# Kernel optimization log

Hardware: AMD Instinct MI355X
Metric: run time of the kernel (lower is better)

Reference implementation:

```python
import jax, jax.numpy as jnp
import numpy as np

def setup_inputs() -> dict:
    key = jax.random.key(0)
    k1, k2 = jax.random.split(key)
    B, S, D, R = 16, 1024, 1024, 128
    batch = jax.random.normal(k1, (B, S, D), dtype=jnp.float32)
    # probe parameter initialized uniform(-0.05, 0.05) as in the torch module
    proj = jax.random.uniform(k2, (D, R), dtype=jnp.float32, minval=-0.05, maxval=0.05)
    return {"batch": batch, "proj": proj}

def reference(batch, proj):
    # transformed: [B, S, R]
    t = jnp.matmul(batch, proj)
    # squared L2 distances for all pairs: ||t_i||^2 + ||t_j||^2 - 2 t_i . t_j
    sq_norms = jnp.sum(t * t, axis=-1)                      # [B, S]
    cross = jnp.einsum('bir,bjr->bij', t, t)                # [B, S, S]
    d = sq_norms[:, :, None] + sq_norms[:, None, :] - 2.0 * cross
    return jnp.maximum(d, 0.0)  # clamp tiny negative values from the identity
```

## Files before the change

### kernel.cpp

```cpp
#include <hip/hip_runtime.h>

typedef __attribute__((ext_vector_type(8))) __bf16 bf16x8;
typedef __attribute__((ext_vector_type(4))) float f32x4;

#define B_ 16
#define S_ 1024
#define D_ 1024
#define R_ 128

__global__ __launch_bounds__(256) void k_transpose(const float* __restrict__ proj,
                                                   __bf16* __restrict__ projT) {
    __shared__ __bf16 tile[64][66];
    const int k0 = blockIdx.x * 64;
    const int r0 = blockIdx.y * 64;
#pragma unroll
    for (int it = 0; it < 16; ++it) {
        int idx = it * 256 + threadIdx.x;
        int kk = idx >> 6, rr = idx & 63;
        tile[kk][rr] = (__bf16)proj[(size_t)(k0 + kk) * R_ + (r0 + rr)];
    }
    __syncthreads();
#pragma unroll
    for (int it = 0; it < 16; ++it) {
        int idx = it * 256 + threadIdx.x;
        int rr = idx >> 6, kk = idx & 63;
        projT[(size_t)(r0 + rr) * D_ + (k0 + kk)] = tile[kk][rr];
    }
}

__global__ __launch_bounds__(256, 4) void k_proj(const float* __restrict__ batch,
                                                 const __bf16* __restrict__ projT,
                                                 __bf16* __restrict__ t,
                                                 float* __restrict__ sqn) {
    const int wave = threadIdx.x >> 6;
    const int lane = threadIdx.x & 63;
    const int ln = lane & 15;
    const int q  = lane >> 4;
    const int m0 = blockIdx.x * 16;
    const int kbase = wave * 256;
    const float* arow = batch + (size_t)(m0 + ln) * D_ + kbase;

    f32x4 acc[8];
#pragma unroll
    for (int ni = 0; ni < 8; ++ni) acc[ni] = f32x4{0.f, 0.f, 0.f, 0.f};

#pragma unroll 4
    for (int k0 = 0; k0 < 256; k0 += 32) {
        const int ka = k0 + q * 8;
        float4 alo = *(const float4*)(arow + ka);
        float4 ahi = *(const float4*)(arow + ka + 4);
        bf16x8 af;
        af[0] = (__bf16)alo.x; af[1] = (__bf16)alo.y;
        af[2] = (__bf16)alo.z; af[3] = (__bf16)alo.w;
        af[4] = (__bf16)ahi.x; af[5] = (__bf16)ahi.y;
        af[6] = (__bf16)ahi.z; af[7] = (__bf16)ahi.w;
#pragma unroll
        for (int ni = 0; ni < 8; ++ni) {
            bf16x8 bf = *(const bf16x8*)(projT + (size_t)(ni * 16 + ln) * D_ + kbase + ka);
            acc[ni] = __builtin_amdgcn_mfma_f32_16x16x32_bf16(af, bf, acc[ni], 0, 0, 0);
        }
    }

    __shared__ f32x4 red[4][8][64];
    __shared__ float sqpart[4][16];
#pragma unroll
    for (int ni = 0; ni < 8; ++ni) red[wave][ni][lane] = acc[ni];
    __syncthreads();

    float sq[4] = {0.f, 0.f, 0.f, 0.f};
#pragma unroll
    for (int p = 0; p < 2; ++p) {
        const int ni = wave * 2 + p;
        f32x4 v = red[0][ni][lane];
#pragma unroll
        for (int w = 1; w < 4; ++w) {
            f32x4 u = red[w][ni][lane];
            v[0] += u[0]; v[1] += u[1]; v[2] += u[2]; v[3] += u[3];
        }
#pragma unroll
        for (int r = 0; r < 4; ++r) {
            __bf16 h = (__bf16)v[r];
            t[(size_t)(m0 + q * 4 + r) * R_ + ni * 16 + ln] = h;
            float f = (float)h;
            sq[r] += f * f;
        }
    }
#pragma unroll
    for (int r = 0; r < 4; ++r) {
#pragma unroll
        for (int off = 1; off < 16; off <<= 1)
            sq[r] += __shfl_xor(sq[r], off, 64);
    }
    if (ln == 0) {
#pragma unroll
        for (int r = 0; r < 4; ++r) sqpart[wave][q * 4 + r] = sq[r];
    }
    __syncthreads();
    if (threadIdx.x < 16) {
        float s = sqpart[0][threadIdx.x] + sqpart[1][threadIdx.x] +
                  sqpart[2][threadIdx.x] + sqpart[3][threadIdx.x];
        sqn[m0 + threadIdx.x] = s;
    }
}

__global__ __launch_bounds__(256) void k_gram(const __bf16* __restrict__ t,
                                              const float* __restrict__ sqn,
                                              float* __restrict__ out) {
    const int b = blockIdx.z;
    const int wave = threadIdx.x >> 6;
    const int lane = threadIdx.x & 63;
    const int ln = lane & 15;
    const int q  = lane >> 4;
    const int wi = wave >> 1, wj = wave & 1;
    const int i0 = blockIdx.y * 128 + wi * 64;
    const int j0 = blockIdx.x * 128 + wj * 64;
    const __bf16* tb = t + (size_t)b * S_ * R_;
    const float* sqb = sqn + (size_t)b * S_;

    f32x4 acc[4][4];
#pragma unroll
    for (int mi = 0; mi < 4; ++mi)
#pragma unroll
        for (int ni = 0; ni < 4; ++ni) acc[mi][ni] = f32x4{0.f, 0.f, 0.f, 0.f};

#pragma unroll
    for (int k0 = 0; k0 < R_; k0 += 32) {
        const int ka = k0 + q * 8;
        bf16x8 af[4], bfm[4];
#pragma unroll
        for (int mi = 0; mi < 4; ++mi)
            af[mi] = *(const bf16x8*)(tb + (size_t)(i0 + mi * 16 + ln) * R_ + ka);
#pragma unroll
        for (int ni = 0; ni < 4; ++ni)
            bfm[ni] = *(const bf16x8*)(tb + (size_t)(j0 + ni * 16 + ln) * R_ + ka);
#pragma unroll
        for (int mi = 0; mi < 4; ++mi)
#pragma unroll
            for (int ni = 0; ni < 4; ++ni)
                acc[mi][ni] = __builtin_amdgcn_mfma_f32_16x16x32_bf16(
                    af[mi], bfm[ni], acc[mi][ni], 0, 0, 0);
    }

    float sqj[4];
#pragma unroll
    for (int ni = 0; ni < 4; ++ni) sqj[ni] = sqb[j0 + ni * 16 + ln];

    float* outb = out + (size_t)b * S_ * S_;
#pragma unroll
    for (int mi = 0; mi < 4; ++mi) {
#pragma unroll
        for (int r = 0; r < 4; ++r) {
            const int i = i0 + mi * 16 + q * 4 + r;
            const float si = sqb[i];
            float* orow = outb + (size_t)i * S_ + j0;
#pragma unroll
            for (int ni = 0; ni < 4; ++ni) {
                float v = si + sqj[ni] - 2.f * acc[mi][ni][r];
                orow[ni * 16 + ln] = fmaxf(v, 0.f);
            }
        }
    }
}

extern "C" void kernel_launch(void* const* d_in, const int* in_sizes, int n_in,
                              void* d_out, int out_size, void* d_ws, size_t ws_size,
                              hipStream_t stream) {
    const float* batch = (const float*)d_in[0];
    const float* proj  = (const float*)d_in[1];
    float* out = (float*)d_out;

    char* ws = (char*)d_ws;
    __bf16* t     = (__bf16*)ws;
    __bf16* projT = (__bf16*)(ws + (size_t)B_ * S_ * R_ * 2);
    float*  sqn   = (float*)(ws + (size_t)B_ * S_ * R_ * 2
                                + (size_t)R_ * D_ * 2);

    k_transpose<<<dim3(D_ / 64, R_ / 64), 256, 0, stream>>>(proj, projT);
    k_proj<<<dim3((B_ * S_) / 16), 256, 0, stream>>>(batch, projT, t, sqn);
    k_gram<<<dim3(S_ / 128, S_ / 128, B_), 256, 0, stream>>>(t, sqn, out);
}
```

Measured before the change: 156.8 us.

## Stage projection inputs through LDS and write gram output transposed as float4

In k_proj, each wave now loads its 16x256 fp32 slice of batch with row-contiguous float4 loads, converts it to bf16 and stages it in shared memory. The MFMA A fragments are then read from LDS, replacing strided per-lane global loads. The reduction buffers reuse the same LDS allocation. k_gram relies on the symmetry of the distance matrix to store each accumulator's four values as one float4 into the transposed position, and gains a launch-bounds occupancy hint; this cuts store instruction count but changes the write access pattern.

Result: no change. 157.5 us (+0.5%).

```diff
diff --git a/kernel.cpp b/kernel.cpp
--- a/kernel.cpp
+++ b/kernel.cpp
@@ -1,6 +1,7 @@
 #include <hip/hip_runtime.h>
 
 typedef __attribute__((ext_vector_type(8))) __bf16 bf16x8;
+typedef __attribute__((ext_vector_type(4))) __bf16 bf16x4;
 typedef __attribute__((ext_vector_type(4))) float f32x4;
 
 #define B_ 16
@@ -28,6 +29,7 @@
     }
 }
 
+#define STG_LD 264
 __global__ __launch_bounds__(256, 4) void k_proj(const float* __restrict__ batch,
                                                  const __bf16* __restrict__ projT,
                                                  __bf16* __restrict__ t,
@@ -38,22 +40,27 @@
     const int q  = lane >> 4;
     const int m0 = blockIdx.x * 16;
     const int kbase = wave * 256;
-    const float* arow = batch + (size_t)(m0 + ln) * D_ + kbase;
+
+    __shared__ __align__(16) char smraw[4 * 16 * STG_LD * 2];
+    __bf16 (*stg)[STG_LD] =
+        reinterpret_cast<__bf16(*)[STG_LD]>(smraw + wave * (16 * STG_LD * 2));
+
+    const float* abase = batch + (size_t)m0 * D_ + kbase;
+#pragma unroll
+    for (int r = 0; r < 16; ++r) {
+        float4 v = *(const float4*)(abase + (size_t)r * D_ + lane * 4);
+        bf16x4 h = {(__bf16)v.x, (__bf16)v.y, (__bf16)v.z, (__bf16)v.w};
+        *(bf16x4*)&stg[r][lane * 4] = h;
+    }
 
     f32x4 acc[8];
 #pragma unroll
     for (int ni = 0; ni < 8; ++ni) acc[ni] = f32x4{0.f, 0.f, 0.f, 0.f};
 
-#pragma unroll 4
+#pragma unroll
     for (int k0 = 0; k0 < 256; k0 += 32) {
         const int ka = k0 + q * 8;
-        float4 alo = *(const float4*)(arow + ka);
-        float4 ahi = *(const float4*)(arow + ka + 4);
-        bf16x8 af;
-        af[0] = (__bf16)alo.x; af[1] = (__bf16)alo.y;
-        af[2] = (__bf16)alo.z; af[3] = (__bf16)alo.w;
-        af[4] = (__bf16)ahi.x; af[5] = (__bf16)ahi.y;
-        af[6] = (__bf16)ahi.z; af[7] = (__bf16)ahi.w;
+        bf16x8 af = *(const bf16x8*)&stg[ln][ka];
 #pragma unroll
         for (int ni = 0; ni < 8; ++ni) {
             bf16x8 bf = *(const bf16x8*)(projT + (size_t)(ni * 16 + ln) * D_ + kbase + ka);
@@ -61,20 +68,21 @@
         }
     }
 
-    __shared__ f32x4 red[4][8][64];
-    __shared__ float sqpart[4][16];
+    __syncthreads();
+    f32x4 (*red)[64] = reinterpret_cast<f32x4(*)[64]>(smraw);
+    float (*sqpart)[16] = reinterpret_cast<float(*)[16]>(smraw + 32768);
 #pragma unroll
-    for (int ni = 0; ni < 8; ++ni) red[wave][ni][lane] = acc[ni];
+    for (int ni = 0; ni < 8; ++ni) red[wave * 8 + ni][lane] = acc[ni];
     __syncthreads();
 
     float sq[4] = {0.f, 0.f, 0.f, 0.f};
 #pragma unroll
     for (int p = 0; p < 2; ++p) {
         const int ni = wave * 2 + p;
-        f32x4 v = red[0][ni][lane];
+        f32x4 v = red[ni][lane];
 #pragma unroll
         for (int w = 1; w < 4; ++w) {
-            f32x4 u = red[w][ni][lane];
+            f32x4 u = red[w * 8 + ni][lane];
             v[0] += u[0]; v[1] += u[1]; v[2] += u[2]; v[3] += u[3];
         }
 #pragma unroll
@@ -103,9 +111,9 @@
     }
 }
 
-__global__ __launch_bounds__(256) void k_gram(const __bf16* __restrict__ t,
-                                              const float* __restrict__ sqn,
-                                              float* __restrict__ out) {
+__global__ __launch_bounds__(256, 4) void k_gram(const __bf16* __restrict__ t,
+                                                 const float* __restrict__ sqn,
+                                                 float* __restrict__ out) {
     const int b = blockIdx.z;
     const int wave = threadIdx.x >> 6;
     const int lane = threadIdx.x & 63;
@@ -148,16 +156,16 @@
     float* outb = out + (size_t)b * S_ * S_;
 #pragma unroll
     for (int mi = 0; mi < 4; ++mi) {
+        float4 si4 = *(const float4*)(sqb + i0 + mi * 16 + q * 4);
 #pragma unroll
-        for (int r = 0; r < 4; ++r) {
-            const int i = i0 + mi * 16 + q * 4 + r;
-            const float si = sqb[i];
-            float* orow = outb + (size_t)i * S_ + j0;
-#pragma unroll
-            for (int ni = 0; ni < 4; ++ni) {
-                float v = si + sqj[ni] - 2.f * acc[mi][ni][r];
-                orow[ni * 16 + ln] = fmaxf(v, 0.f);
-            }
+        for (int ni = 0; ni < 4; ++ni) {
+            const int j = j0 + ni * 16 + ln;
+            float4 o;
+            o.x = fmaxf(si4.x + sqj[ni] - 2.f * acc[mi][ni][0], 0.f);
+            o.y = fmaxf(si4.y + sqj[ni] - 2.f * acc[mi][ni][1], 0.f);
+            o.z = fmaxf(si4.z + sqj[ni] - 2.f * acc[mi][ni][2], 0.f);
+            o.w = fmaxf(si4.w + sqj[ni] - 2.f * acc[mi][ni][3], 0.f);
+            *(float4*)(outb + (size_t)j * S_ + i0 + mi * 16 + q * 4) = o;
         }
     }
 }
```
